# Performance work log

Measured on AMD Instinct MI355X. Metric: run time of the kernel, lower is better.

Reference implementation:

```python
import jax, jax.numpy as jnp
import numpy as np

LEAK = 0.01   # nn.LeakyReLU default negative_slope
EPS = 1e-5    # BatchNorm eps

D, H, W = 32, 480, 480
N = 200000
CIN, COUT = 64, 128


def _neighbor_table(z, y, x, order, sorted_flat, offsets):
    # For each kernel offset, index of the active voxel at (z+dz, y+dy, x+dx), or -1.
    n = z.shape[0]
    tabs = []
    for dz, dy, dx in offsets:
        nz, ny, nx = z + dz, y + dy, x + dx
        valid = (nz >= 0) & (nz < D) & (ny >= 0) & (ny < H) & (nx >= 0) & (nx < W)
        nflat = (nz * H + ny) * W + nx
        pos = np.searchsorted(sorted_flat, nflat).clip(0, n - 1)
        found = valid & (sorted_flat[pos] == nflat)
        tabs.append(np.where(found, order[pos], -1).astype(np.int32))
    return np.stack(tabs)  # [9, N]


def setup_inputs() -> dict:
    rng = np.random.default_rng(0)
    flat = rng.choice(D * H * W, N, replace=False).astype(np.int64)
    z = flat // (H * W)
    y = (flat // W) % H
    x = flat % W
    order = np.argsort(flat)
    sorted_flat = flat[order]
    off133 = [(0, dy, dx) for dy in (-1, 0, 1) for dx in (-1, 0, 1)]  # kernel (1,3,3)
    off313 = [(dz, 0, dx) for dz in (-1, 0, 1) for dx in (-1, 0, 1)]  # kernel (3,1,3)
    nbr133 = jnp.asarray(_neighbor_table(z, y, x, order, sorted_flat, off133))
    nbr313 = jnp.asarray(_neighbor_table(z, y, x, order, sorted_flat, off313))

    key = jax.random.key(0)
    ks = jax.random.split(key, 14)
    feats = jax.random.normal(ks[0], (N, CIN), jnp.float32)
    # SubMConv3d weights, flattened kernel volume first: [9, Cin, Cout]
    W00 = jax.random.normal(ks[1], (9, CIN, COUT), jnp.float32) * 0.05   # conv0_0 (1,3,3)
    W01 = jax.random.normal(ks[2], (9, COUT, COUT), jnp.float32) * 0.05  # conv0_1 (3,1,3)
    W10 = jax.random.normal(ks[3], (9, CIN, COUT), jnp.float32) * 0.05   # conv1_0 (3,1,3)
    W11 = jax.random.normal(ks[4], (9, COUT, COUT), jnp.float32) * 0.05  # conv1_1 (1,3,3)

    def bn_params(k):
        k1, k2, k3, k4 = jax.random.split(k, 4)
        gamma = 1.0 + 0.1 * jax.random.normal(k1, (COUT,), jnp.float32)
        beta = 0.1 * jax.random.normal(k2, (COUT,), jnp.float32)
        mean = 0.1 * jax.random.normal(k3, (COUT,), jnp.float32)
        var = jax.random.uniform(k4, (COUT,), jnp.float32, 0.5, 1.5)
        return jnp.stack([gamma, beta, mean, var])  # [4, Cout]

    return {
        'feats': feats,
        'W00': W00, 'W01': W01, 'W10': W10, 'W11': W11,
        'bn00': bn_params(ks[5]), 'bn01': bn_params(ks[6]),
        'bn10': bn_params(ks[7]), 'bn11': bn_params(ks[8]),
        'nbr133': nbr133, 'nbr313': nbr313,
    }


def _subm_conv(f, nbr, Wk):
    # Rulebook gather-matmul-accumulate: out[n] = sum_k f[nbr[k, n]] @ Wk[k]
    out = jnp.zeros((f.shape[0], Wk.shape[2]), f.dtype)
    for k in range(Wk.shape[0]):  # 9 fixed kernel offsets
        idx = nbr[k]
        valid = idx >= 0
        g = jnp.where(valid[:, None], f[jnp.where(valid, idx, 0)], 0.0)
        out = out + g @ Wk[k]
    return out


def _act_bn(x, p):
    # LeakyReLU then BatchNorm (eval: running stats), matching forward order
    x = jnp.where(x >= 0, x, LEAK * x)
    scale = p[0] * jax.lax.rsqrt(p[3] + EPS)
    return (x - p[2]) * scale + p[1]


def reference(feats, W00, W01, W10, W11, bn00, bn01, bn10, bn11, nbr133, nbr313):
    shortcut = _act_bn(_subm_conv(feats, nbr133, W00), bn00)
    shortcut = _act_bn(_subm_conv(shortcut, nbr313, W01), bn01)
    res = _act_bn(_subm_conv(feats, nbr313, W10), bn10)
    res = _act_bn(_subm_conv(res, nbr133, W11), bn11)
    return res + shortcut
```

## Files before the change

kernel.cpp:

```cpp
#include <hip/hip_runtime.h>
#include <hip/hip_bf16.h>

#define LEAK 0.01f
#define BN_EPS 1e-5f
#define CAP_P 8192

using frag_b16 = __attribute__((ext_vector_type(8))) short;
using f32x4    = __attribute__((ext_vector_type(4))) float;

union U4F { uint4 u; frag_b16 f; };

__device__ __forceinline__ float bf2f(unsigned short u) {
    union { unsigned int i; float f; } v;
    v.i = ((unsigned int)u) << 16;
    return v.f;
}

__device__ __forceinline__ unsigned short f2bf(float f) {
    union { float f; unsigned int i; } v;
    v.f = f;
    unsigned int u = v.i;
    return (unsigned short)((u + 0x7fffu + ((u >> 16) & 1u)) >> 16);
}

__device__ __forceinline__ unsigned int pk_bf16(float lo, float hi) {
    __hip_bfloat162 h = __float22bfloat162_rn(make_float2(lo, hi));
    union { __hip_bfloat162 h; unsigned int u; } c;
    c.h = h;
    return c.u;
}

__global__ __launch_bounds__(256) void transpose_all(
    const float* __restrict__ w0, const float* __restrict__ w1,
    const float* __restrict__ w2, const float* __restrict__ w3,
    const float* __restrict__ b0, const float* __restrict__ b1,
    const float* __restrict__ b2, const float* __restrict__ b3,
    unsigned short* __restrict__ o0, unsigned short* __restrict__ o1,
    unsigned short* __restrict__ o2, unsigned short* __restrict__ o3,
    float* __restrict__ scsh) {
    const int t64 = 9 * 64 * 128, t128 = 9 * 128 * 128;
    int i = blockIdx.x * 256 + threadIdx.x;
    const float* w; unsigned short* o; int cin;
    if (i < t64)                        { w = w0; o = o0; cin = 64; }
    else if ((i -= t64) < t128)         { w = w1; o = o1; cin = 128; }
    else if ((i -= t128) < t64)         { w = w2; o = o2; cin = 64; }
    else if ((i -= t64) < t128)         { w = w3; o = o3; cin = 128; }
    else if ((i -= t128) < 512) {
        int conv = i >> 7, c = i & 127;
        const float* bn = (conv == 0) ? b0 : (conv == 1) ? b1 : (conv == 2) ? b2 : b3;
        float s = bn[c] * rsqrtf(bn[384 + c] + BN_EPS);
        scsh[conv * 256 + c] = s;
        scsh[conv * 256 + 128 + c] = bn[128 + c] - bn[256 + c] * s;
        return;
    }
    else return;
    int co = i & 127;
    int rest = i >> 7;
    int ci = rest % cin;
    int k = rest / cin;
    o[((size_t)k * 128 + co) * cin + ci] = f2bf(w[i]);
}

__global__ __launch_bounds__(256) void rules_count(
    const int* __restrict__ nbrA, const int* __restrict__ nbrB,
    int N, int NB, int* __restrict__ blockCnt) {
    __shared__ int cnts[16][4];
    const int tid = threadIdx.x, lane = tid & 63, wave = tid >> 6;
    const int n = blockIdx.x * 256 + tid;
    #pragma unroll
    for (int c = 0; c < 16; ++c) {
        const int* nb = (c < 8) ? nbrA : nbrB;
        int j = c & 7;
        int k = j + (j >= 4);
        int v = (n < N) ? nb[(size_t)k * N + n] : -1;
        unsigned long long m = __ballot(v >= 0);
        if (lane == 0) cnts[c][wave] = __popcll(m);
    }
    __syncthreads();
    if (tid < 16)
        blockCnt[tid * NB + blockIdx.x] =
            cnts[tid][0] + cnts[tid][1] + cnts[tid][2] + cnts[tid][3];
}

__global__ __launch_bounds__(1024) void rules_scan(
    const int* __restrict__ blockCnt, int NB,
    int* __restrict__ blockBase, int* __restrict__ meta) {
    const int lane = threadIdx.x & 63, w = threadIdx.x >> 6;
    int running = 0;
    for (int base = 0; base < NB; base += 64) {
        int i = base + lane;
        int v = (i < NB) ? blockCnt[w * NB + i] : 0;
        int s = v;
        #pragma unroll
        for (int d = 1; d < 64; d <<= 1) {
            int t = __shfl_up(s, d);
            if (lane >= d) s += t;
        }
        if (i < NB) blockBase[w * NB + i] = running + s - v;
        running += __shfl(s, 63);
    }
    if (lane == 0) meta[w] = running;
}

__global__ __launch_bounds__(256) void rules_fill(
    const int* __restrict__ nbrA, const int* __restrict__ nbrB,
    int N, int NB, const int* __restrict__ blockBase,
    int* __restrict__ pairsAll, int* __restrict__ ptabA, int* __restrict__ ptabB) {
    __shared__ int wcnt[16][4];
    __shared__ int wpre[16][4];
    const int tid = threadIdx.x, lane = tid & 63, wave = tid >> 6;
    const int n = blockIdx.x * 256 + tid;
    int vv[16], rk[16];
    #pragma unroll
    for (int c = 0; c < 16; ++c) {
        const int* nb = (c < 8) ? nbrA : nbrB;
        int j = c & 7;
        int k = j + (j >= 4);
        int v = (n < N) ? nb[(size_t)k * N + n] : -1;
        vv[c] = v;
        unsigned long long m = __ballot(v >= 0);
        rk[c] = (int)__popcll(m & ((1ull << lane) - 1ull));
        if (lane == 0) wcnt[c][wave] = (int)__popcll(m);
    }
    __syncthreads();
    if (tid < 16) {
        int s = 0;
        #pragma unroll
        for (int w = 0; w < 4; ++w) { wpre[tid][w] = s; s += wcnt[tid][w]; }
    }
    __syncthreads();
    if (n < N) {
        #pragma unroll
        for (int c = 0; c < 16; ++c) {
            int j = c & 7;
            int* ptab = (c < 8) ? ptabA : ptabB;
            int idx = -1;
            if (vv[c] >= 0) {
                idx = blockBase[c * NB + blockIdx.x] + wpre[c][wave] + rk[c];
                if (idx < CAP_P) pairsAll[c * CAP_P + idx] = vv[c];
                else idx = -1;
            }
            ptab[(size_t)n * 8 + j] = idx;
        }
    }
}


template <int CIN, bool IN_F32>
__global__ __launch_bounds__(256) void pairs_fused(
    const void* __restrict__ finA, const void* __restrict__ finB,
    const int*  __restrict__ pairsAll,
    const int*  __restrict__ meta,
    const unsigned short* __restrict__ wtA,
    const unsigned short* __restrict__ wtB,
    unsigned short* __restrict__ contribLo,
    unsigned short* __restrict__ contribHi,
    int pairXor) {
    const int job = blockIdx.y;
    const int j = job & 7, k = j + (j >= 4);
    const bool second = job >= 8;
    const void* fin = second ? finB : finA;
    const unsigned short* wk = (second ? wtB : wtA) + (size_t)k * 128 * CIN;
    unsigned short* ctb = (second ? contribHi : contribLo) + (size_t)j * CAP_P * 128;
    const int pidx = job ^ pairXor;
    const int* pairs = pairsAll + (size_t)pidx * CAP_P;
    const int cnt = min(meta[pidx], CAP_P);
    const int wave = threadIdx.x >> 6, lane = threadIdx.x & 63;
    const int l16 = lane & 15, quad = lane >> 4;
    const int pbase = (blockIdx.x * 4 + wave) * 16;
    if (pbase >= cnt) return;
    const int p = pbase + l16;
    const int inrow = (p < cnt) ? pairs[p] : -1;

    f32x4 acc[8] = {};
    #pragma unroll
    for (int c = 0; c < CIN / 32; ++c) {
        U4F u;
        u.u = make_uint4(0u, 0u, 0u, 0u);
        if (inrow >= 0) {
            if (IN_F32) {
                const float* fp = (const float*)fin;
                const float4* p4 = (const float4*)(fp + (size_t)inrow * CIN + c * 32 + quad * 8);
                float4 a = p4[0], b = p4[1];
                u.u.x = pk_bf16(a.x, a.y); u.u.y = pk_bf16(a.z, a.w);
                u.u.z = pk_bf16(b.x, b.y); u.u.w = pk_bf16(b.z, b.w);
            } else {
                u.u = *(const uint4*)((const unsigned short*)fin + (size_t)inrow * CIN + c * 32 + quad * 8);
            }
        }
        frag_b16 bfr = u.f;
        #pragma unroll
        for (int ni = 0; ni < 8; ++ni) {
            frag_b16 afr = *(const frag_b16*)(wk + (size_t)(ni * 16 + l16) * CIN + c * 32 + quad * 8);
            acc[ni] = __builtin_amdgcn_mfma_f32_16x16x32_bf16(afr, bfr, acc[ni], 0, 0, 0);
        }
    }
    if (p < cnt) {
        unsigned short* cr = ctb + (size_t)p * 128 + quad * 4;
        #pragma unroll
        for (int ni = 0; ni < 8; ++ni) {
            uint2 o;
            o.x = pk_bf16(acc[ni][0], acc[ni][1]);
            o.y = pk_bf16(acc[ni][2], acc[ni][3]);
            *(uint2*)(cr + ni * 16) = o;
        }
    }
}

__global__ __launch_bounds__(256, 3) void convK1(
    const float* __restrict__ feats,
    const unsigned short* __restrict__ wt00,
    const unsigned short* __restrict__ wt10,
    const int* __restrict__ ptab133,
    const int* __restrict__ ptab313,
    const unsigned short* __restrict__ contribLo,
    const unsigned short* __restrict__ contribHi,
    const float* __restrict__ scsh,
    unsigned short* __restrict__ s1,
    unsigned short* __restrict__ r1,
    int N) {
    const int tid = threadIdx.x, lane = tid & 63, wave = tid >> 6;
    const int waveM = wave >> 1, waveN = wave & 1;
    const int l16 = lane & 15, quad = lane >> 4;
    const int n0 = blockIdx.x * 64;
    const unsigned short* wS = wt00 + (size_t)4 * 128 * 64;
    const unsigned short* wR = wt10 + (size_t)4 * 128 * 64;

    f32x4 accS[2][4] = {}, accR[2][4] = {};
    #pragma unroll
    for (int c = 0; c < 2; ++c) {
        frag_b16 bF[2];
        #pragma unroll
        for (int mi = 0; mi < 2; ++mi) {
            int n = n0 + waveM * 32 + mi * 16 + l16;
            U4F u;
            u.u = make_uint4(0u, 0u, 0u, 0u);
            if (n < N) {
                const float4* p4 = (const float4*)(feats + (size_t)n * 64 + c * 32 + quad * 8);
                float4 a = p4[0], b = p4[1];
                u.u.x = pk_bf16(a.x, a.y); u.u.y = pk_bf16(a.z, a.w);
                u.u.z = pk_bf16(b.x, b.y); u.u.w = pk_bf16(b.z, b.w);
            }
            bF[mi] = u.f;
        }
        #pragma unroll
        for (int ni = 0; ni < 4; ++ni) {
            frag_b16 aS = *(const frag_b16*)(wS + (size_t)(waveN * 64 + ni * 16 + l16) * 64 + c * 32 + quad * 8);
            frag_b16 aR = *(const frag_b16*)(wR + (size_t)(waveN * 64 + ni * 16 + l16) * 64 + c * 32 + quad * 8);
            #pragma unroll
            for (int mi = 0; mi < 2; ++mi) {
                accS[mi][ni] = __builtin_amdgcn_mfma_f32_16x16x32_bf16(aS, bF[mi], accS[mi][ni], 0, 0, 0);
                accR[mi][ni] = __builtin_amdgcn_mfma_f32_16x16x32_bf16(aR, bF[mi], accR[mi][ni], 0, 0, 0);
            }
        }
    }

    const int cOff = waveN * 64 + quad * 4;
    #pragma unroll
    for (int mi = 0; mi < 2; ++mi) {
        int n = n0 + waveM * 32 + mi * 16 + l16;
        if (n >= N) continue;
        f32x4 mS[4] = {}, mR[4] = {};
        const int4* ptS4 = (const int4*)(ptab133 + (size_t)n * 8);
        const int4* ptR4 = (const int4*)(ptab313 + (size_t)n * 8);
        int4 sa = ptS4[0], sb = ptS4[1];
        int4 ra = ptR4[0], rb = ptR4[1];
        int pjS[8] = {sa.x, sa.y, sa.z, sa.w, sb.x, sb.y, sb.z, sb.w};
        int pjR[8] = {ra.x, ra.y, ra.z, ra.w, rb.x, rb.y, rb.z, rb.w};
        #pragma unroll
        for (int j = 0; j < 8; ++j) {
            if (pjS[j] >= 0) {
                const unsigned short* cr = contribLo + ((size_t)j * CAP_P + pjS[j]) * 128 + cOff;
                #pragma unroll
                for (int ni = 0; ni < 4; ++ni) {
                    uint2 v = *(const uint2*)(cr + ni * 16);
                    mS[ni][0] += bf2f((unsigned short)(v.x & 0xffffu));
                    mS[ni][1] += bf2f((unsigned short)(v.x >> 16));
                    mS[ni][2] += bf2f((unsigned short)(v.y & 0xffffu));
                    mS[ni][3] += bf2f((unsigned short)(v.y >> 16));
                }
            }
            if (pjR[j] >= 0) {
                const unsigned short* cr = contribHi + ((size_t)j * CAP_P + pjR[j]) * 128 + cOff;
                #pragma unroll
                for (int ni = 0; ni < 4; ++ni) {
                    uint2 v = *(const uint2*)(cr + ni * 16);
                    mR[ni][0] += bf2f((unsigned short)(v.x & 0xffffu));
                    mR[ni][1] += bf2f((unsigned short)(v.x >> 16));
                    mR[ni][2] += bf2f((unsigned short)(v.y & 0xffffu));
                    mR[ni][3] += bf2f((unsigned short)(v.y >> 16));
                }
            }
        }
        #pragma unroll
        for (int ni = 0; ni < 4; ++ni) {
            int c = cOff + ni * 16;
            f32x4 scS = *(const f32x4*)(scsh + c);
            f32x4 shS = *(const f32x4*)(scsh + 128 + c);
            f32x4 scR = *(const f32x4*)(scsh + 512 + c);
            f32x4 shR = *(const f32x4*)(scsh + 512 + 128 + c);
            float vs[4], vr[4];
            #pragma unroll
            for (int r = 0; r < 4; ++r) {
                float xs = accS[mi][ni][r] + mS[ni][r];
                xs = (xs >= 0.0f) ? xs : LEAK * xs;
                vs[r] = xs * scS[r] + shS[r];
                float xr = accR[mi][ni][r] + mR[ni][r];
                xr = (xr >= 0.0f) ? xr : LEAK * xr;
                vr[r] = xr * scR[r] + shR[r];
            }
            uint2 oS, oR;
            oS.x = pk_bf16(vs[0], vs[1]); oS.y = pk_bf16(vs[2], vs[3]);
            oR.x = pk_bf16(vr[0], vr[1]); oR.y = pk_bf16(vr[2], vr[3]);
            *(uint2*)(s1 + (size_t)n * 128 + c) = oS;
            *(uint2*)(r1 + (size_t)n * 128 + c) = oR;
        }
    }
}

__global__ __launch_bounds__(256, 3) void convK2(
    const unsigned short* __restrict__ s1,
    const unsigned short* __restrict__ r1,
    const unsigned short* __restrict__ wt01,
    const unsigned short* __restrict__ wt11,
    const int* __restrict__ ptab313,
    const int* __restrict__ ptab133,
    const unsigned short* __restrict__ contribLo,
    const unsigned short* __restrict__ contribHi,
    const float* __restrict__ scsh,
    float* __restrict__ out, int N) {
    const int tid = threadIdx.x, lane = tid & 63, wave = tid >> 6;
    const int waveM = wave >> 1, waveN = wave & 1;
    const int l16 = lane & 15, quad = lane >> 4;
    const int n0 = blockIdx.x * 64;
    const unsigned short* wS = wt01 + (size_t)4 * 128 * 128;
    const unsigned short* wR = wt11 + (size_t)4 * 128 * 128;

    f32x4 accS[2][4] = {}, accR[2][4] = {};
    #pragma unroll
    for (int c = 0; c < 4; ++c) {
        frag_b16 bS[2], bR[2];
        #pragma unroll
        for (int mi = 0; mi < 2; ++mi) {
            int n = n0 + waveM * 32 + mi * 16 + l16;
            U4F us, ur;
            us.u = make_uint4(0u, 0u, 0u, 0u);
            ur.u = us.u;
            if (n < N) {
                us.u = *(const uint4*)(s1 + (size_t)n * 128 + c * 32 + quad * 8);
                ur.u = *(const uint4*)(r1 + (size_t)n * 128 + c * 32 + quad * 8);
            }
            bS[mi] = us.f;
            bR[mi] = ur.f;
        }
        #pragma unroll
        for (int ni = 0; ni < 4; ++ni) {
            frag_b16 aS = *(const frag_b16*)(wS + (size_t)(waveN * 64 + ni * 16 + l16) * 128 + c * 32 + quad * 8);
            frag_b16 aR = *(const frag_b16*)(wR + (size_t)(waveN * 64 + ni * 16 + l16) * 128 + c * 32 + quad * 8);
            #pragma unroll
            for (int mi = 0; mi < 2; ++mi) {
                accS[mi][ni] = __builtin_amdgcn_mfma_f32_16x16x32_bf16(aS, bS[mi], accS[mi][ni], 0, 0, 0);
                accR[mi][ni] = __builtin_amdgcn_mfma_f32_16x16x32_bf16(aR, bR[mi], accR[mi][ni], 0, 0, 0);
            }
        }
    }

    const int cOff = waveN * 64 + quad * 4;
    #pragma unroll
    for (int mi = 0; mi < 2; ++mi) {
        int n = n0 + waveM * 32 + mi * 16 + l16;
        if (n >= N) continue;
        f32x4 mS[4] = {}, mR[4] = {};
        const int4* ptS4 = (const int4*)(ptab313 + (size_t)n * 8);
        const int4* ptR4 = (const int4*)(ptab133 + (size_t)n * 8);
        int4 sa = ptS4[0], sb = ptS4[1];
        int4 ra = ptR4[0], rb = ptR4[1];
        int pjS[8] = {sa.x, sa.y, sa.z, sa.w, sb.x, sb.y, sb.z, sb.w};
        int pjR[8] = {ra.x, ra.y, ra.z, ra.w, rb.x, rb.y, rb.z, rb.w};
        #pragma unroll
        for (int j = 0; j < 8; ++j) {
            if (pjS[j] >= 0) {
                const unsigned short* cr = contribLo + ((size_t)j * CAP_P + pjS[j]) * 128 + cOff;
                #pragma unroll
                for (int ni = 0; ni < 4; ++ni) {
                    uint2 v = *(const uint2*)(cr + ni * 16);
                    mS[ni][0] += bf2f((unsigned short)(v.x & 0xffffu));
                    mS[ni][1] += bf2f((unsigned short)(v.x >> 16));
                    mS[ni][2] += bf2f((unsigned short)(v.y & 0xffffu));
                    mS[ni][3] += bf2f((unsigned short)(v.y >> 16));
                }
            }
            if (pjR[j] >= 0) {
                const unsigned short* cr = contribHi + ((size_t)j * CAP_P + pjR[j]) * 128 + cOff;
                #pragma unroll
                for (int ni = 0; ni < 4; ++ni) {
                    uint2 v = *(const uint2*)(cr + ni * 16);
                    mR[ni][0] += bf2f((unsigned short)(v.x & 0xffffu));
                    mR[ni][1] += bf2f((unsigned short)(v.x >> 16));
                    mR[ni][2] += bf2f((unsigned short)(v.y & 0xffffu));
                    mR[ni][3] += bf2f((unsigned short)(v.y >> 16));
                }
            }
        }
        #pragma unroll
        for (int ni = 0; ni < 4; ++ni) {
            int c = cOff + ni * 16;
            f32x4 sc1 = *(const f32x4*)(scsh + 256 + c);
            f32x4 sh1 = *(const f32x4*)(scsh + 256 + 128 + c);
            f32x4 sc3 = *(const f32x4*)(scsh + 768 + c);
            f32x4 sh3 = *(const f32x4*)(scsh + 768 + 128 + c);
            f32x4 o;
            #pragma unroll
            for (int r = 0; r < 4; ++r) {
                float xs = accS[mi][ni][r] + mS[ni][r];
                xs = (xs >= 0.0f) ? xs : LEAK * xs;
                xs = xs * sc1[r] + sh1[r];
                float xr = accR[mi][ni][r] + mR[ni][r];
                xr = (xr >= 0.0f) ? xr : LEAK * xr;
                xr = xr * sc3[r] + sh3[r];
                o[r] = xr + xs;
            }
            *(f32x4*)(out + (size_t)n * 128 + c) = o;
        }
    }
}


template <int CIN, bool IN_F32>
__global__ __launch_bounds__(256) void pairs_gemm2(
    const void* __restrict__ fin_,
    const int*  __restrict__ pairsT,
    const int*  __restrict__ metaT,
    const unsigned short* __restrict__ wt,
    unsigned short* __restrict__ contrib) {
    const int j = blockIdx.y;
    const int k = j + (j >= 4);
    const int cnt = min(metaT[j], CAP_P);
    const int wave = threadIdx.x >> 6, lane = threadIdx.x & 63;
    const int base = (blockIdx.x * 4 + wave) * 16;
    if (base >= cnt) return;
    const int l16 = lane & 15, quad = lane >> 4;
    const int p = base + l16;
    const int inrow = (p < cnt) ? pairsT[j * CAP_P + p] : -1;
    const unsigned short* wk = wt + (size_t)k * 128 * CIN;

    f32x4 acc[8] = {};
    #pragma unroll
    for (int c = 0; c < CIN / 32; ++c) {
        U4F u;
        u.u = make_uint4(0u, 0u, 0u, 0u);
        if (inrow >= 0) {
            if (IN_F32) {
                const float* fin = (const float*)fin_;
                const float4* p4 = (const float4*)(fin + (size_t)inrow * CIN + c * 32 + quad * 8);
                float4 a = p4[0], b = p4[1];
                u.u.x = pk_bf16(a.x, a.y); u.u.y = pk_bf16(a.z, a.w);
                u.u.z = pk_bf16(b.x, b.y); u.u.w = pk_bf16(b.z, b.w);
            } else {
                u.u = *(const uint4*)((const unsigned short*)fin_ + (size_t)inrow * CIN + c * 32 + quad * 8);
            }
        }
        frag_b16 af = u.f;
        #pragma unroll
        for (int ni = 0; ni < 8; ++ni) {
            frag_b16 bf = *(const frag_b16*)(wk + (ni * 16 + l16) * CIN + c * 32 + quad * 8);
            acc[ni] = __builtin_amdgcn_mfma_f32_16x16x32_bf16(af, bf, acc[ni], 0, 0, 0);
        }
    }
    unsigned short* cj = contrib + ((size_t)j * CAP_P + base) * 128;
    #pragma unroll
    for (int r = 0; r < 4; ++r) {
        int row = quad * 4 + r;
        #pragma unroll
        for (int ni = 0; ni < 8; ++ni)
            cj[(size_t)row * 128 + ni * 16 + l16] = f2bf(acc[ni][r]);
    }
}

template <int CIN, bool IN_F32, bool OUT_BF16, int ADDMODE>
__global__ __launch_bounds__(256, 4) void conv_center3(
    const void* __restrict__ fin_,
    const unsigned short* __restrict__ wt,
    const int*  __restrict__ ptabT,
    const unsigned short* __restrict__ contrib,
    const float* __restrict__ bn,
    const unsigned short* __restrict__ addbf,
    void* __restrict__ out_,
    int N) {
    const int tid = threadIdx.x;
    const int lane = tid & 63;
    const int wave = tid >> 6;
    const int waveM = wave >> 1, waveN = wave & 1;
    const int l16 = lane & 15, quad = lane >> 4;
    const int n0 = blockIdx.x * 64;
    const unsigned short* wc = wt + (size_t)4 * 128 * CIN;

    f32x4 acc[2][4] = {};
    #pragma unroll
    for (int c = 0; c < CIN / 32; ++c) {
        frag_b16 bf[4], af[2];
        #pragma unroll
        for (int ni = 0; ni < 4; ++ni)
            bf[ni] = *(const frag_b16*)(wc + (waveN * 64 + ni * 16 + l16) * CIN + c * 32 + quad * 8);
        #pragma unroll
        for (int mi = 0; mi < 2; ++mi) {
            int n = n0 + waveM * 32 + mi * 16 + l16;
            U4F u;
            u.u = make_uint4(0u, 0u, 0u, 0u);
            if (n < N) {
                if (IN_F32) {
                    const float* fin = (const float*)fin_;
                    const float4* p4 = (const float4*)(fin + (size_t)n * CIN + c * 32 + quad * 8);
                    float4 a = p4[0], b = p4[1];
                    u.u.x = pk_bf16(a.x, a.y); u.u.y = pk_bf16(a.z, a.w);
                    u.u.z = pk_bf16(b.x, b.y); u.u.w = pk_bf16(b.z, b.w);
                } else {
                    u.u = *(const uint4*)((const unsigned short*)fin_ + (size_t)n * CIN + c * 32 + quad * 8);
                }
            }
            af[mi] = u.f;
        }
        #pragma unroll
        for (int mi = 0; mi < 2; ++mi)
            #pragma unroll
            for (int ni = 0; ni < 4; ++ni)
                acc[mi][ni] = __builtin_amdgcn_mfma_f32_16x16x32_bf16(af[mi], bf[ni], acc[mi][ni], 0, 0, 0);
    }

    float sc[4], sh[4];
    int col[4];
    #pragma unroll
    for (int ni = 0; ni < 4; ++ni) {
        int c = waveN * 64 + ni * 16 + l16;
        col[ni] = c;
        float s = bn[c] * rsqrtf(bn[384 + c] + BN_EPS);
        sc[ni] = s;
        sh[ni] = bn[128 + c] - bn[256 + c] * s;
    }
    #pragma unroll
    for (int mi = 0; mi < 2; ++mi) {
        int rbase = n0 + waveM * 32 + mi * 16 + quad * 4;
        #pragma unroll
        for (int r = 0; r < 4; ++r) {
            int n = rbase + r;
            if (n < N) {
                const int4* pt = (const int4*)(ptabT + (size_t)n * 8);
                int4 pa = pt[0], pb = pt[1];
                int pj[8] = {pa.x, pa.y, pa.z, pa.w, pb.x, pb.y, pb.z, pb.w};
                float m[4] = {0.f, 0.f, 0.f, 0.f};
                #pragma unroll
                for (int j = 0; j < 8; ++j) {
                    int pi = pj[j];
                    if (pi >= 0) {
                        const unsigned short* cr = contrib + ((size_t)j * CAP_P + pi) * 128;
                        #pragma unroll
                        for (int ni = 0; ni < 4; ++ni) m[ni] += bf2f(cr[col[ni]]);
                    }
                }
                float addv[4] = {0.f, 0.f, 0.f, 0.f};
                if (ADDMODE == 1) {
                    #pragma unroll
                    for (int ni = 0; ni < 4; ++ni)
                        addv[ni] = bf2f(addbf[(size_t)n * 128 + col[ni]]);
                } else if (ADDMODE == 2) {
                    #pragma unroll
                    for (int ni = 0; ni < 4; ++ni)
                        addv[ni] = ((const float*)out_)[(size_t)n * 128 + col[ni]];
                }
                #pragma unroll
                for (int ni = 0; ni < 4; ++ni) {
                    float x = acc[mi][ni][r] + m[ni];
                    x = (x >= 0.0f) ? x : LEAK * x;
                    x = x * sc[ni] + sh[ni];
                    x += addv[ni];
                    if (OUT_BF16)
                        ((unsigned short*)out_)[(size_t)n * 128 + col[ni]] = f2bf(x);
                    else
                        ((float*)out_)[(size_t)n * 128 + col[ni]] = x;
                }
            }
        }
    }
}

template <int CIN, bool IN_F32, bool OUT_F32, bool ADD>
__global__ __launch_bounds__(256) void conv_mfma(
    const void*  __restrict__ fin_,
    const int*   __restrict__ nbr,
    const unsigned short* __restrict__ wt,
    const float* __restrict__ bn,
    const float* __restrict__ addsrc,
    void*        __restrict__ out_,
    int N) {
    constexpr int SEGS = CIN / 8;
    constexpr int RPP = 256 / SEGS;
    constexpr int PASSES = 128 / RPP;
    __shared__ unsigned short ldsA[128 * CIN];
    __shared__ unsigned short ldsW[128 * CIN];
    const int tid = threadIdx.x;
    const int lane = tid & 63;
    const int wave = tid >> 6;
    const int waveM = wave >> 1, waveN = wave & 1;
    const int l16 = lane & 15, quad = lane >> 4;
    const int n0 = blockIdx.x * 128;
    const int srow = tid / SEGS, sseg = tid % SEGS;
    f32x4 acc[4][4] = {};
    for (int k = 0; k < 9; ++k) {
        if (k) __syncthreads();
        #pragma unroll
        for (int p = 0; p < PASSES; ++p) {
            int r = p * RPP + srow;
            int n = n0 + r;
            int idx = (n < N) ? nbr[(size_t)k * N + n] : -1;
            uint4 v = make_uint4(0u, 0u, 0u, 0u);
            if (IN_F32) {
                const float* fin = (const float*)fin_;
                float4 a = make_float4(0.f, 0.f, 0.f, 0.f);
                float4 b = make_float4(0.f, 0.f, 0.f, 0.f);
                if (idx >= 0) {
                    const float4* p4 = (const float4*)(fin + (size_t)idx * CIN) + sseg * 2;
                    a = p4[0]; b = p4[1];
                }
                v.x = pk_bf16(a.x, a.y); v.y = pk_bf16(a.z, a.w);
                v.z = pk_bf16(b.x, b.y); v.w = pk_bf16(b.z, b.w);
            } else {
                const unsigned short* fin = (const unsigned short*)fin_;
                if (idx >= 0) v = *((const uint4*)(fin + (size_t)idx * CIN) + sseg);
            }
            *(uint4*)(ldsA + r * CIN + ((sseg ^ (r & 7)) << 3)) = v;
        }
        const unsigned short* wk = wt + (size_t)k * 128 * CIN;
        #pragma unroll
        for (int p = 0; p < PASSES; ++p) {
            int r = p * RPP + srow;
            *(uint4*)(ldsW + r * CIN + ((sseg ^ (r & 7)) << 3)) =
                *((const uint4*)(wk + r * CIN) + sseg);
        }
        __syncthreads();
        #pragma unroll
        for (int c = 0; c < CIN / 32; ++c) {
            frag_b16 af[4], bf[4];
            #pragma unroll
            for (int i = 0; i < 4; ++i) {
                int seg = (c * 4 + quad) ^ (l16 & 7);
                af[i] = *(const frag_b16*)(ldsA + (waveM * 64 + i * 16 + l16) * CIN + (seg << 3));
                bf[i] = *(const frag_b16*)(ldsW + (waveN * 64 + i * 16 + l16) * CIN + (seg << 3));
            }
            #pragma unroll
            for (int mi = 0; mi < 4; ++mi)
                #pragma unroll
                for (int ni = 0; ni < 4; ++ni)
                    acc[mi][ni] = __builtin_amdgcn_mfma_f32_16x16x32_bf16(af[mi], bf[ni], acc[mi][ni], 0, 0, 0);
        }
    }
    float sc[4], sh[4];
    int col[4];
    #pragma unroll
    for (int ni = 0; ni < 4; ++ni) {
        int c = waveN * 64 + ni * 16 + l16;
        col[ni] = c;
        float s = bn[c] * rsqrtf(bn[384 + c] + BN_EPS);
        sc[ni] = s;
        sh[ni] = bn[128 + c] - bn[256 + c] * s;
    }
    #pragma unroll
    for (int mi = 0; mi < 4; ++mi) {
        int rbase = n0 + waveM * 64 + mi * 16 + quad * 4;
        #pragma unroll
        for (int r = 0; r < 4; ++r) {
            int n = rbase + r;
            if (n < N) {
                #pragma unroll
                for (int ni = 0; ni < 4; ++ni) {
                    float x = acc[mi][ni][r];
                    x = (x >= 0.0f) ? x : LEAK * x;
                    x = x * sc[ni] + sh[ni];
                    if (ADD) x += addsrc[(size_t)n * 128 + col[ni]];
                    if (OUT_F32) ((float*)out_)[(size_t)n * 128 + col[ni]] = x;
                    else ((unsigned short*)out_)[(size_t)n * 128 + col[ni]] = f2bf(x);
                }
            }
        }
    }
}

extern "C" void kernel_launch(void* const* d_in, const int* in_sizes, int n_in,
                              void* d_out, int out_size, void* d_ws, size_t ws_size,
                              hipStream_t stream) {
    const float* feats = (const float*)d_in[0];
    const float* W00 = (const float*)d_in[1];
    const float* W01 = (const float*)d_in[2];
    const float* W10 = (const float*)d_in[3];
    const float* W11 = (const float*)d_in[4];
    const float* bn00 = (const float*)d_in[5];
    const float* bn01 = (const float*)d_in[6];
    const float* bn10 = (const float*)d_in[7];
    const float* bn11 = (const float*)d_in[8];
    const int* nbr133 = (const int*)d_in[9];
    const int* nbr313 = (const int*)d_in[10];
    const int N = in_sizes[0] / 64;
    const int NB = (N + 255) / 256;

    char* ws = (char*)d_ws;
    size_t off = 0;
    auto alloc = [&](size_t bytes) -> char* {
        char* p = ws + off;
        off = (off + bytes + 255) & ~(size_t)255;
        return p;
    };
    unsigned short* bufA = (unsigned short*)alloc((size_t)N * 128 * 2);
    unsigned short* wt00 = (unsigned short*)alloc(9 * 128 * 64 * 2);
    unsigned short* wt01 = (unsigned short*)alloc(9 * 128 * 128 * 2);
    unsigned short* wt10 = (unsigned short*)alloc(9 * 128 * 64 * 2);
    unsigned short* wt11 = (unsigned short*)alloc(9 * 128 * 128 * 2);
    float* scsh = (float*)alloc(4 * 2 * 128 * 4);
    int* ptab133 = (int*)alloc((size_t)N * 8 * 4);
    int* ptab313 = (int*)alloc((size_t)N * 8 * 4);
    int* pairsAll = (int*)alloc((size_t)16 * CAP_P * 4);
    int* blockCnt = (int*)alloc((size_t)16 * NB * 4);
    int* blockBase = (int*)alloc((size_t)16 * NB * 4);
    int* meta = (int*)alloc(16 * 4);
    unsigned short* contribLo = (unsigned short*)alloc((size_t)8 * CAP_P * 128 * 2);
    const size_t offTierB = off;
    unsigned short* bufB = (unsigned short*)alloc((size_t)N * 128 * 2);
    const size_t offTierA = off;
    unsigned short* contribHi = (unsigned short*)alloc((size_t)8 * CAP_P * 128 * 2);
    const size_t offFused = off;

    const bool fusedOk = (ws_size >= offFused);
    const bool tierA = (ws_size >= offTierA);
    const bool tierB = (ws_size >= offTierB);

    const int totalW = 2 * (9 * 64 * 128) + 2 * (9 * 128 * 128);
    hipLaunchKernelGGL(transpose_all, dim3((totalW + 512 + 255) / 256), dim3(256), 0, stream,
                       W00, W01, W10, W11, bn00, bn01, bn10, bn11,
                       wt00, wt01, wt10, wt11, scsh);

    float* outF = (float*)d_out;
    const int cblocks = (N + 63) / 64;

    if (fusedOk) {
        hipLaunchKernelGGL(rules_count, dim3(NB), dim3(256), 0, stream,
                           nbr133, nbr313, N, NB, blockCnt);
        hipLaunchKernelGGL(rules_scan, dim3(1), dim3(1024), 0, stream,
                           blockCnt, NB, blockBase, meta);
        hipLaunchKernelGGL(rules_fill, dim3(NB), dim3(256), 0, stream,
                           nbr133, nbr313, N, NB, blockBase, pairsAll, ptab133, ptab313);

        const dim3 pg(CAP_P / 64, 16);
        hipLaunchKernelGGL((pairs_fused<64, true>), pg, dim3(256), 0, stream,
                           (const void*)feats, (const void*)feats, pairsAll, meta,
                           wt00, wt10, contribLo, contribHi, 0);
        hipLaunchKernelGGL(convK1, dim3(cblocks), dim3(256), 0, stream,
                           feats, wt00, wt10, ptab133, ptab313,
                           contribLo, contribHi, scsh, bufA, bufB, N);
        hipLaunchKernelGGL((pairs_fused<128, false>), pg, dim3(256), 0, stream,
                           (const void*)bufA, (const void*)bufB, pairsAll, meta,
                           wt01, wt11, contribLo, contribHi, 8);
        hipLaunchKernelGGL(convK2, dim3(cblocks), dim3(256), 0, stream,
                           bufA, bufB, wt01, wt11, ptab313, ptab133,
                           contribLo, contribHi, scsh, outF, N);
    } else if (tierA || tierB) {
        hipLaunchKernelGGL(rules_count, dim3(NB), dim3(256), 0, stream,
                           nbr133, nbr313, N, NB, blockCnt);
        hipLaunchKernelGGL(rules_scan, dim3(1), dim3(1024), 0, stream,
                           blockCnt, NB, blockBase, meta);
        hipLaunchKernelGGL(rules_fill, dim3(NB), dim3(256), 0, stream,
                           nbr133, nbr313, N, NB, blockBase, pairsAll, ptab133, ptab313);

        const dim3 pg(CAP_P / 64, 8);
        const int* pairs133 = pairsAll;
        const int* pairs313 = pairsAll + 8 * CAP_P;
        const int* meta133 = meta;
        const int* meta313 = meta + 8;
        const unsigned short* nullbf = nullptr;

        hipLaunchKernelGGL((pairs_gemm2<64, true>), pg, dim3(256), 0, stream,
                           (const void*)feats, pairs133, meta133, wt00, contribLo);
        hipLaunchKernelGGL((conv_center3<64, true, true, 0>), dim3(cblocks), dim3(256), 0, stream,
                           (const void*)feats, wt00, ptab133, contribLo, bn00, nullbf, (void*)bufA, N);
        hipLaunchKernelGGL((pairs_gemm2<128, false>), pg, dim3(256), 0, stream,
                           (const void*)bufA, pairs313, meta313, wt01, contribLo);
        if (tierA)
            hipLaunchKernelGGL((conv_center3<128, false, true, 0>), dim3(cblocks), dim3(256), 0, stream,
                               (const void*)bufA, wt01, ptab313, contribLo, bn01, nullbf, (void*)bufB, N);
        else
            hipLaunchKernelGGL((conv_center3<128, false, false, 0>), dim3(cblocks), dim3(256), 0, stream,
                               (const void*)bufA, wt01, ptab313, contribLo, bn01, nullbf, (void*)outF, N);
        hipLaunchKernelGGL((pairs_gemm2<64, true>), pg, dim3(256), 0, stream,
                           (const void*)feats, pairs313, meta313, wt10, contribLo);
        hipLaunchKernelGGL((conv_center3<64, true, true, 0>), dim3(cblocks), dim3(256), 0, stream,
                           (const void*)feats, wt10, ptab313, contribLo, bn10, nullbf, (void*)bufA, N);
        hipLaunchKernelGGL((pairs_gemm2<128, false>), pg, dim3(256), 0, stream,
                           (const void*)bufA, pairs133, meta133, wt11, contribLo);
        if (tierA)
            hipLaunchKernelGGL((conv_center3<128, false, false, 1>), dim3(cblocks), dim3(256), 0, stream,
                               (const void*)bufA, wt11, ptab133, contribLo, bn11, bufB, (void*)outF, N);
        else
            hipLaunchKernelGGL((conv_center3<128, false, false, 2>), dim3(cblocks), dim3(256), 0, stream,
                               (const void*)bufA, wt11, ptab133, contribLo, bn11, nullbf, (void*)outF, N);
    } else {
        const int blocks = (N + 127) / 128;
        hipLaunchKernelGGL((conv_mfma<64, true, false, false>), dim3(blocks), dim3(256), 0, stream,
                           (const void*)feats, nbr133, wt00, bn00, (const float*)nullptr, (void*)bufA, N);
        hipLaunchKernelGGL((conv_mfma<128, false, true, false>), dim3(blocks), dim3(256), 0, stream,
                           (const void*)bufA, nbr313, wt01, bn01, (const float*)nullptr, (void*)outF, N);
        hipLaunchKernelGGL((conv_mfma<64, true, false, false>), dim3(blocks), dim3(256), 0, stream,
                           (const void*)feats, nbr313, wt10, bn10, (const float*)nullptr, (void*)bufA, N);
        hipLaunchKernelGGL((conv_mfma<128, false, true, true>), dim3(blocks), dim3(256), 0, stream,
                           (const void*)bufA, nbr133, wt11, bn11, outF, (void*)outF, N);
    }
}
```

Measured before the change: 460.3 us.

## Pack neighbor pair lists compactly, shrink conv tiles, pre-convert feats to bf16

Replaces the per-voxel 8-int pair tables with a packed 16-byte list of valid (offset, pair index) entries, so the center conv kernels read one uint4 and loop only over present neighbors instead of checking eight entries. The fused conv kernels now process 32 voxels per block with higher occupancy (launch bounds 4) and do the neighbor merge before the MFMA loop. When workspace allows, feats are converted once to bf16 so the pair GEMM and first center conv read half the bytes. This costs an extra conversion kernel and restructured workspace allocation, and halves per-block weight reuse.

```diff
diff --git a/kernel.cpp b/kernel.cpp
--- a/kernel.cpp
+++ b/kernel.cpp
@@ -61,6 +61,18 @@
     o[((size_t)k * 128 + co) * cin + ci] = f2bf(w[i]);
 }
 
+__global__ __launch_bounds__(256) void feats_to_bf16(
+    const float* __restrict__ f, unsigned short* __restrict__ o, int total8) {
+    int i = blockIdx.x * 256 + threadIdx.x;
+    if (i >= total8) return;
+    const float4* p4 = (const float4*)(f + (size_t)i * 8);
+    float4 a = p4[0], b = p4[1];
+    uint4 u;
+    u.x = pk_bf16(a.x, a.y); u.y = pk_bf16(a.z, a.w);
+    u.z = pk_bf16(b.x, b.y); u.w = pk_bf16(b.z, b.w);
+    ((uint4*)o)[i] = u;
+}
+
 __global__ __launch_bounds__(256) void rules_count(
     const int* __restrict__ nbrA, const int* __restrict__ nbrB,
     int N, int NB, int* __restrict__ blockCnt) {
@@ -105,7 +117,9 @@
 __global__ __launch_bounds__(256) void rules_fill(
     const int* __restrict__ nbrA, const int* __restrict__ nbrB,
     int N, int NB, const int* __restrict__ blockBase,
-    int* __restrict__ pairsAll, int* __restrict__ ptabA, int* __restrict__ ptabB) {
+    int* __restrict__ pairsAll,
+    int* __restrict__ ptabA, int* __restrict__ ptabB,
+    uint4* __restrict__ pakA, uint4* __restrict__ pakB) {
     __shared__ int wcnt[16][4];
     __shared__ int wpre[16][4];
     const int tid = threadIdx.x, lane = tid & 63, wave = tid >> 6;
@@ -130,18 +144,42 @@
     }
     __syncthreads();
     if (n < N) {
+        unsigned long long la0 = ~0ull, la1 = ~0ull, lb0 = ~0ull, lb1 = ~0ull;
+        int na = 0, nbp = 0;
         #pragma unroll
         for (int c = 0; c < 16; ++c) {
             int j = c & 7;
-            int* ptab = (c < 8) ? ptabA : ptabB;
             int idx = -1;
             if (vv[c] >= 0) {
                 idx = blockBase[c * NB + blockIdx.x] + wpre[c][wave] + rk[c];
                 if (idx < CAP_P) pairsAll[c * CAP_P + idx] = vv[c];
                 else idx = -1;
             }
-            ptab[(size_t)n * 8 + j] = idx;
-        }
+            if (c < 8) { if (ptabA) ptabA[(size_t)n * 8 + j] = idx; }
+            else       { if (ptabB) ptabB[(size_t)n * 8 + j] = idx; }
+            if (idx >= 0) {
+                unsigned e = ((unsigned)j << 13) | (unsigned)idx;
+                if (e != 0xFFFFu) {
+                    if (c < 8) {
+                        int s = (na & 3) * 16;
+                        unsigned long long m = 0xFFFFull << s;
+                        unsigned long long ev = (unsigned long long)e << s;
+                        if (na < 4) la0 = (la0 & ~m) | ev; else la1 = (la1 & ~m) | ev;
+                        ++na;
+                    } else {
+                        int s = (nbp & 3) * 16;
+                        unsigned long long m = 0xFFFFull << s;
+                        unsigned long long ev = (unsigned long long)e << s;
+                        if (nbp < 4) lb0 = (lb0 & ~m) | ev; else lb1 = (lb1 & ~m) | ev;
+                        ++nbp;
+                    }
+                }
+            }
+        }
+        if (pakA) pakA[n] = make_uint4((unsigned)la0, (unsigned)(la0 >> 32),
+                                       (unsigned)la1, (unsigned)(la1 >> 32));
+        if (pakB) pakB[n] = make_uint4((unsigned)lb0, (unsigned)(lb0 >> 32),
+                                       (unsigned)lb1, (unsigned)(lb1 >> 32));
     }
 }
 
@@ -207,12 +245,35 @@
     }
 }
 
-__global__ __launch_bounds__(256, 3) void convK1(
-    const float* __restrict__ feats,
+__device__ __forceinline__ void merge_gather(
+    uint4 pk, const unsigned short* __restrict__ contrib, int cOff, f32x4 (&acc)[4]) {
+    if (pk.x == 0xFFFFFFFFu) return;
+    unsigned long long lo = ((unsigned long long)pk.y << 32) | pk.x;
+    unsigned long long hi = ((unsigned long long)pk.w << 32) | pk.z;
+    #pragma unroll 1
+    for (int t = 0; t < 8; ++t) {
+        unsigned v = (unsigned)(((t < 4) ? lo : hi) >> ((t & 3) << 4)) & 0xFFFFu;
+        if (v == 0xFFFFu) break;
+        const unsigned short* cr =
+            contrib + ((size_t)(v >> 13) * CAP_P + (v & 0x1FFFu)) * 128 + cOff;
+        #pragma unroll
+        for (int ni = 0; ni < 4; ++ni) {
+            uint2 g = *(const uint2*)(cr + ni * 16);
+            acc[ni][0] += bf2f((unsigned short)(g.x & 0xffffu));
+            acc[ni][1] += bf2f((unsigned short)(g.x >> 16));
+            acc[ni][2] += bf2f((unsigned short)(g.y & 0xffffu));
+            acc[ni][3] += bf2f((unsigned short)(g.y >> 16));
+        }
+    }
+}
+
+template <bool IN_F32>
+__global__ __launch_bounds__(256, 4) void convK1(
+    const void* __restrict__ feats_,
     const unsigned short* __restrict__ wt00,
     const unsigned short* __restrict__ wt10,
-    const int* __restrict__ ptab133,
-    const int* __restrict__ ptab313,
+    const uint4* __restrict__ pakA,
+    const uint4* __restrict__ pakB,
     const unsigned short* __restrict__ contribLo,
     const unsigned short* __restrict__ contribHi,
     const float* __restrict__ scsh,
@@ -222,90 +283,56 @@
     const int tid = threadIdx.x, lane = tid & 63, wave = tid >> 6;
     const int waveM = wave >> 1, waveN = wave & 1;
     const int l16 = lane & 15, quad = lane >> 4;
-    const int n0 = blockIdx.x * 64;
+    const int n = blockIdx.x * 32 + waveM * 16 + l16;
+    const bool live = (n < N);
     const unsigned short* wS = wt00 + (size_t)4 * 128 * 64;
     const unsigned short* wR = wt10 + (size_t)4 * 128 * 64;
-
-    f32x4 accS[2][4] = {}, accR[2][4] = {};
+    const int cOff = waveN * 64 + quad * 4;
+
+    f32x4 accS[4] = {}, accR[4] = {};
+    if (live) {
+        merge_gather(pakA[n], contribLo, cOff, accS);
+        merge_gather(pakB[n], contribHi, cOff, accR);
+    }
     #pragma unroll
     for (int c = 0; c < 2; ++c) {
-        frag_b16 bF[2];
-        #pragma unroll
-        for (int mi = 0; mi < 2; ++mi) {
-            int n = n0 + waveM * 32 + mi * 16 + l16;
-            U4F u;
-            u.u = make_uint4(0u, 0u, 0u, 0u);
-            if (n < N) {
-                const float4* p4 = (const float4*)(feats + (size_t)n * 64 + c * 32 + quad * 8);
+        U4F u;
+        u.u = make_uint4(0u, 0u, 0u, 0u);
+        if (live) {
+            if (IN_F32) {
+                const float* fp = (const float*)feats_;
+                const float4* p4 = (const float4*)(fp + (size_t)n * 64 + c * 32 + quad * 8);
                 float4 a = p4[0], b = p4[1];
                 u.u.x = pk_bf16(a.x, a.y); u.u.y = pk_bf16(a.z, a.w);
                 u.u.z = pk_bf16(b.x, b.y); u.u.w = pk_bf16(b.z, b.w);
-            }
-            bF[mi] = u.f;
-        }
+            } else {
+                u.u = *(const uint4*)((const unsigned short*)feats_ + (size_t)n * 64 + c * 32 + quad * 8);
+            }
+        }
+        frag_b16 bIn = u.f;
         #pragma unroll
         for (int ni = 0; ni < 4; ++ni) {
             frag_b16 aS = *(const frag_b16*)(wS + (size_t)(waveN * 64 + ni * 16 + l16) * 64 + c * 32 + quad * 8);
             frag_b16 aR = *(const frag_b16*)(wR + (size_t)(waveN * 64 + ni * 16 + l16) * 64 + c * 32 + quad * 8);
-            #pragma unroll
-            for (int mi = 0; mi < 2; ++mi) {
-                accS[mi][ni] = __builtin_amdgcn_mfma_f32_16x16x32_bf16(aS, bF[mi], accS[mi][ni], 0, 0, 0);
-                accR[mi][ni] = __builtin_amdgcn_mfma_f32_16x16x32_bf16(aR, bF[mi], accR[mi][ni], 0, 0, 0);
-            }
-        }
-    }
-
-    const int cOff = waveN * 64 + quad * 4;
-    #pragma unroll
-    for (int mi = 0; mi < 2; ++mi) {
-        int n = n0 + waveM * 32 + mi * 16 + l16;
-        if (n >= N) continue;
-        f32x4 mS[4] = {}, mR[4] = {};
-        const int4* ptS4 = (const int4*)(ptab133 + (size_t)n * 8);
-        const int4* ptR4 = (const int4*)(ptab313 + (size_t)n * 8);
-        int4 sa = ptS4[0], sb = ptS4[1];
-        int4 ra = ptR4[0], rb = ptR4[1];
-        int pjS[8] = {sa.x, sa.y, sa.z, sa.w, sb.x, sb.y, sb.z, sb.w};
-        int pjR[8] = {ra.x, ra.y, ra.z, ra.w, rb.x, rb.y, rb.z, rb.w};
-        #pragma unroll
-        for (int j = 0; j < 8; ++j) {
-            if (pjS[j] >= 0) {
-                const unsigned short* cr = contribLo + ((size_t)j * CAP_P + pjS[j]) * 128 + cOff;
-                #pragma unroll
-                for (int ni = 0; ni < 4; ++ni) {
-                    uint2 v = *(const uint2*)(cr + ni * 16);
-                    mS[ni][0] += bf2f((unsigned short)(v.x & 0xffffu));
-                    mS[ni][1] += bf2f((unsigned short)(v.x >> 16));
-                    mS[ni][2] += bf2f((unsigned short)(v.y & 0xffffu));
-                    mS[ni][3] += bf2f((unsigned short)(v.y >> 16));
-                }
-            }
-            if (pjR[j] >= 0) {
-                const unsigned short* cr = contribHi + ((size_t)j * CAP_P + pjR[j]) * 128 + cOff;
-                #pragma unroll
-                for (int ni = 0; ni < 4; ++ni) {
-                    uint2 v = *(const uint2*)(cr + ni * 16);
-                    mR[ni][0] += bf2f((unsigned short)(v.x & 0xffffu));
-                    mR[ni][1] += bf2f((unsigned short)(v.x >> 16));
-                    mR[ni][2] += bf2f((unsigned short)(v.y & 0xffffu));
-                    mR[ni][3] += bf2f((unsigned short)(v.y >> 16));
-                }
-            }
-        }
+            accS[ni] = __builtin_amdgcn_mfma_f32_16x16x32_bf16(aS, bIn, accS[ni], 0, 0, 0);
+            accR[ni] = __builtin_amdgcn_mfma_f32_16x16x32_bf16(aR, bIn, accR[ni], 0, 0, 0);
+        }
+    }
+    if (live) {
         #pragma unroll
         for (int ni = 0; ni < 4; ++ni) {
             int c = cOff + ni * 16;
             f32x4 scS = *(const f32x4*)(scsh + c);
             f32x4 shS = *(const f32x4*)(scsh + 128 + c);
             f32x4 scR = *(const f32x4*)(scsh + 512 + c);
-            f32x4 shR = *(const f32x4*)(scsh + 512 + 128 + c);
+            f32x4 shR = *(const f32x4*)(scsh + 640 + c);
             float vs[4], vr[4];
             #pragma unroll
             for (int r = 0; r < 4; ++r) {
-                float xs = accS[mi][ni][r] + mS[ni][r];
+                float xs = accS[ni][r];
                 xs = (xs >= 0.0f) ? xs : LEAK * xs;
                 vs[r] = xs * scS[r] + shS[r];
-                float xr = accR[mi][ni][r] + mR[ni][r];
+                float xr = accR[ni][r];
                 xr = (xr >= 0.0f) ? xr : LEAK * xr;
                 vr[r] = xr * scR[r] + shR[r];
             }
@@ -318,13 +345,13 @@
     }
 }
 
-__global__ __launch_bounds__(256, 3) void convK2(
+__global__ __launch_bounds__(256, 4) void convK2(
     const unsigned short* __restrict__ s1,
     const unsigned short* __restrict__ r1,
     const unsigned short* __restrict__ wt01,
     const unsigned short* __restrict__ wt11,
-    const int* __restrict__ ptab313,
-    const int* __restrict__ ptab133,
+    const uint4* __restrict__ pakB,
+    const uint4* __restrict__ pakA,
     const unsigned short* __restrict__ contribLo,
     const unsigned short* __restrict__ contribHi,
     const float* __restrict__ scsh,
@@ -332,90 +359,50 @@
     const int tid = threadIdx.x, lane = tid & 63, wave = tid >> 6;
     const int waveM = wave >> 1, waveN = wave & 1;
     const int l16 = lane & 15, quad = lane >> 4;
-    const int n0 = blockIdx.x * 64;
+    const int n = blockIdx.x * 32 + waveM * 16 + l16;
+    const bool live = (n < N);
     const unsigned short* wS = wt01 + (size_t)4 * 128 * 128;
     const unsigned short* wR = wt11 + (size_t)4 * 128 * 128;
-
-    f32x4 accS[2][4] = {}, accR[2][4] = {};
+    const int cOff = waveN * 64 + quad * 4;
+
+    f32x4 accS[4] = {}, accR[4] = {};
+    if (live) {
+        merge_gather(pakB[n], contribLo, cOff, accS);
+        merge_gather(pakA[n], contribHi, cOff, accR);
+    }
     #pragma unroll
     for (int c = 0; c < 4; ++c) {
-        frag_b16 bS[2], bR[2];
-        #pragma unroll
-        for (int mi = 0; mi < 2; ++mi) {
-            int n = n0 + waveM * 32 + mi * 16 + l16;
-            U4F us, ur;
-            us.u = make_uint4(0u, 0u, 0u, 0u);
-            ur.u = us.u;
-            if (n < N) {
-                us.u = *(const uint4*)(s1 + (size_t)n * 128 + c * 32 + quad * 8);
-                ur.u = *(const uint4*)(r1 + (size_t)n * 128 + c * 32 + quad * 8);
-            }
-            bS[mi] = us.f;
-            bR[mi] = ur.f;
-        }
+        U4F us, ur;
+        us.u = make_uint4(0u, 0u, 0u, 0u);
+        ur.u = us.u;
+        if (live) {
+            us.u = *(const uint4*)(s1 + (size_t)n * 128 + c * 32 + quad * 8);
+            ur.u = *(const uint4*)(r1 + (size_t)n * 128 + c * 32 + quad * 8);
+        }
+        frag_b16 bS = us.f, bR = ur.f;
         #pragma unroll
         for (int ni = 0; ni < 4; ++ni) {
             frag_b16 aS = *(const frag_b16*)(wS + (size_t)(waveN * 64 + ni * 16 + l16) * 128 + c * 32 + quad * 8);
             frag_b16 aR = *(const frag_b16*)(wR + (size_t)(waveN * 64 + ni * 16 + l16) * 128 + c * 32 + quad * 8);
-            #pragma unroll
-            for (int mi = 0; mi < 2; ++mi) {
-                accS[mi][ni] = __builtin_amdgcn_mfma_f32_16x16x32_bf16(aS, bS[mi], accS[mi][ni], 0, 0, 0);
-                accR[mi][ni] = __builtin_amdgcn_mfma_f32_16x16x32_bf16(aR, bR[mi], accR[mi][ni], 0, 0, 0);
-            }
-        }
-    }
-
-    const int cOff = waveN * 64 + quad * 4;
-    #pragma unroll
-    for (int mi = 0; mi < 2; ++mi) {
-        int n = n0 + waveM * 32 + mi * 16 + l16;
-        if (n >= N) continue;
-        f32x4 mS[4] = {}, mR[4] = {};
-        const int4* ptS4 = (const int4*)(ptab313 + (size_t)n * 8);
-        const int4* ptR4 = (const int4*)(ptab133 + (size_t)n * 8);
-        int4 sa = ptS4[0], sb = ptS4[1];
-        int4 ra = ptR4[0], rb = ptR4[1];
-        int pjS[8] = {sa.x, sa.y, sa.z, sa.w, sb.x, sb.y, sb.z, sb.w};
-        int pjR[8] = {ra.x, ra.y, ra.z, ra.w, rb.x, rb.y, rb.z, rb.w};
-        #pragma unroll
-        for (int j = 0; j < 8; ++j) {
-            if (pjS[j] >= 0) {
-                const unsigned short* cr = contribLo + ((size_t)j * CAP_P + pjS[j]) * 128 + cOff;
-                #pragma unroll
-                for (int ni = 0; ni < 4; ++ni) {
-                    uint2 v = *(const uint2*)(cr + ni * 16);
-                    mS[ni][0] += bf2f((unsigned short)(v.x & 0xffffu));
-                    mS[ni][1] += bf2f((unsigned short)(v.x >> 16));
-                    mS[ni][2] += bf2f((unsigned short)(v.y & 0xffffu));
-                    mS[ni][3] += bf2f((unsigned short)(v.y >> 16));
-                }
-            }
-            if (pjR[j] >= 0) {
-                const unsigned short* cr = contribHi + ((size_t)j * CAP_P + pjR[j]) * 128 + cOff;
-                #pragma unroll
-                for (int ni = 0; ni < 4; ++ni) {
-                    uint2 v = *(const uint2*)(cr + ni * 16);
-                    mR[ni][0] += bf2f((unsigned short)(v.x & 0xffffu));
-                    mR[ni][1] += bf2f((unsigned short)(v.x >> 16));
-                    mR[ni][2] += bf2f((unsigned short)(v.y & 0xffffu));
-                    mR[ni][3] += bf2f((unsigned short)(v.y >> 16));
-                }
-            }
-        }
+            accS[ni] = __builtin_amdgcn_mfma_f32_16x16x32_bf16(aS, bS, accS[ni], 0, 0, 0);
+            accR[ni] = __builtin_amdgcn_mfma_f32_16x16x32_bf16(aR, bR, accR[ni], 0, 0, 0);
+        }
+    }
+    if (live) {
         #pragma unroll
         for (int ni = 0; ni < 4; ++ni) {
             int c = cOff + ni * 16;
             f32x4 sc1 = *(const f32x4*)(scsh + 256 + c);
-            f32x4 sh1 = *(const f32x4*)(scsh + 256 + 128 + c);
+            f32x4 sh1 = *(const f32x4*)(scsh + 384 + c);
             f32x4 sc3 = *(const f32x4*)(scsh + 768 + c);
-            f32x4 sh3 = *(const f32x4*)(scsh + 768 + 128 + c);
+            f32x4 sh3 = *(const f32x4*)(scsh + 896 + c);
             f32x4 o;
             #pragma unroll
             for (int r = 0; r < 4; ++r) {
-                float xs = accS[mi][ni][r] + mS[ni][r];
+                float xs = accS[ni][r];
                 xs = (xs >= 0.0f) ? xs : LEAK * xs;
                 xs = xs * sc1[r] + sh1[r];
-                float xr = accR[mi][ni][r] + mR[ni][r];
+                float xr = accR[ni][r];
                 xr = (xr >= 0.0f) ? xr : LEAK * xr;
                 xr = xr * sc3[r] + sh3[r];
                 o[r] = xr + xs;
@@ -714,20 +701,30 @@
     unsigned short* wt10 = (unsigned short*)alloc(9 * 128 * 64 * 2);
     unsigned short* wt11 = (unsigned short*)alloc(9 * 128 * 128 * 2);
     float* scsh = (float*)alloc(4 * 2 * 128 * 4);
-    int* ptab133 = (int*)alloc((size_t)N * 8 * 4);
-    int* ptab313 = (int*)alloc((size_t)N * 8 * 4);
     int* pairsAll = (int*)alloc((size_t)16 * CAP_P * 4);
     int* blockCnt = (int*)alloc((size_t)16 * NB * 4);
     int* blockBase = (int*)alloc((size_t)16 * NB * 4);
     int* meta = (int*)alloc(16 * 4);
     unsigned short* contribLo = (unsigned short*)alloc((size_t)8 * CAP_P * 128 * 2);
-    const size_t offTierB = off;
+    const size_t offX = off;
+
+    uint4* pakA = (uint4*)alloc((size_t)N * 16);
+    uint4* pakB = (uint4*)alloc((size_t)N * 16);
     unsigned short* bufB = (unsigned short*)alloc((size_t)N * 128 * 2);
-    const size_t offTierA = off;
     unsigned short* contribHi = (unsigned short*)alloc((size_t)8 * CAP_P * 128 * 2);
     const size_t offFused = off;
+    unsigned short* feats16 = (unsigned short*)alloc((size_t)N * 64 * 2);
+    const size_t offFusedF16 = off;
+
+    off = offX;
+    int* ptab133 = (int*)alloc((size_t)N * 8 * 4);
+    int* ptab313 = (int*)alloc((size_t)N * 8 * 4);
+    const size_t offTierB = off;
+    unsigned short* bufB_t = (unsigned short*)alloc((size_t)N * 128 * 2);
+    const size_t offTierA = off;
 
     const bool fusedOk = (ws_size >= offFused);
+    const bool useF16 = (ws_size >= offFusedF16);
     const bool tierA = (ws_size >= offTierA);
     const bool tierB = (ws_size >= offTierB);
 
@@ -737,28 +734,43 @@
                        wt00, wt01, wt10, wt11, scsh);
 
     float* outF = (float*)d_out;
-    const int cblocks = (N + 63) / 64;
 
     if (fusedOk) {
+        if (useF16) {
+            const int total8 = N * 8;
+            hipLaunchKernelGGL(feats_to_bf16, dim3((total8 + 255) / 256), dim3(256), 0, stream,
+                               feats, feats16, total8);
+        }
         hipLaunchKernelGGL(rules_count, dim3(NB), dim3(256), 0, stream,
                            nbr133, nbr313, N, NB, blockCnt);
         hipLaunchKernelGGL(rules_scan, dim3(1), dim3(1024), 0, stream,
                            blockCnt, NB, blockBase, meta);
         hipLaunchKernelGGL(rules_fill, dim3(NB), dim3(256), 0, stream,
-                           nbr133, nbr313, N, NB, blockBase, pairsAll, ptab133, ptab313);
+                           nbr133, nbr313, N, NB, blockBase, pairsAll,
+                           (int*)nullptr, (int*)nullptr, pakA, pakB);
 
         const dim3 pg(CAP_P / 64, 16);
-        hipLaunchKernelGGL((pairs_fused<64, true>), pg, dim3(256), 0, stream,
-                           (const void*)feats, (const void*)feats, pairsAll, meta,
-                           wt00, wt10, contribLo, contribHi, 0);
-        hipLaunchKernelGGL(convK1, dim3(cblocks), dim3(256), 0, stream,
-                           feats, wt00, wt10, ptab133, ptab313,
-                           contribLo, contribHi, scsh, bufA, bufB, N);
+        const int kblocks = (N + 31) / 32;
+        if (useF16) {
+            hipLaunchKernelGGL((pairs_fused<64, false>), pg, dim3(256), 0, stream,
+                               (const void*)feats16, (const void*)feats16, pairsAll, meta,
+                               wt00, wt10, contribLo, contribHi, 0);
+            hipLaunchKernelGGL((convK1<false>), dim3(kblocks), dim3(256), 0, stream,
+                               (const void*)feats16, wt00, wt10, pakA, pakB,
+                               contribLo, contribHi, scsh, bufA, bufB, N);
+        } else {
+            hipLaunchKernelGGL((pairs_fused<64, true>), pg, dim3(256), 0, stream,
+                               (const void*)feats, (const void*)feats, pairsAll, meta,
+                               wt00, wt10, contribLo, contribHi, 0);
+            hipLaunchKernelGGL((convK1<true>), dim3(kblocks), dim3(256), 0, stream,
+                               (const void*)feats, wt00, wt10, pakA, pakB,
+                               contribLo, contribHi, scsh, bufA, bufB, N);
+        }
         hipLaunchKernelGGL((pairs_fused<128, false>), pg, dim3(256), 0, stream,
                            (const void*)bufA, (const void*)bufB, pairsAll, meta,
                            wt01, wt11, contribLo, contribHi, 8);
-        hipLaunchKernelGGL(convK2, dim3(cblocks), dim3(256), 0, stream,
-                           bufA, bufB, wt01, wt11, ptab313, ptab133,
+        hipLaunchKernelGGL(convK2, dim3(kblocks), dim3(256), 0, stream,
+                           bufA, bufB, wt01, wt11, pakB, pakA,
                            contribLo, contribHi, scsh, outF, N);
     } else if (tierA || tierB) {
         hipLaunchKernelGGL(rules_count, dim3(NB), dim3(256), 0, stream,
@@ -766,7 +778,8 @@
         hipLaunchKernelGGL(rules_scan, dim3(1), dim3(1024), 0, stream,
                            blockCnt, NB, blockBase, meta);
         hipLaunchKernelGGL(rules_fill, dim3(NB), dim3(256), 0, stream,
-                           nbr133, nbr313, N, NB, blockBase, pairsAll, ptab133, ptab313);
+                           nbr133, nbr313, N, NB, blockBase, pairsAll,
+                           ptab133, ptab313, (uint4*)nullptr, (uint4*)nullptr);
 
         const dim3 pg(CAP_P / 64, 8);
         const int* pairs133 = pairsAll;
@@ -774,6 +787,7 @@
         const int* meta133 = meta;
         const int* meta313 = meta + 8;
         const unsigned short* nullbf = nullptr;
+        const int cblocks = (N + 63) / 64;
 
         hipLaunchKernelGGL((pairs_gemm2<64, true>), pg, dim3(256), 0, stream,
                            (const void*)feats, pairs133, meta133, wt00, contribLo);
@@ -783,7 +797,7 @@
                            (const void*)bufA, pairs313, meta313, wt01, contribLo);
         if (tierA)
             hipLaunchKernelGGL((conv_center3<128, false, true, 0>), dim3(cblocks), dim3(256), 0, stream,
-                               (const void*)bufA, wt01, ptab313, contribLo, bn01, nullbf, (void*)bufB, N);
+                               (const void*)bufA, wt01, ptab313, contribLo, bn01, nullbf, (void*)bufB_t, N);
         else
             hipLaunchKernelGGL((conv_center3<128, false, false, 0>), dim3(cblocks), dim3(256), 0, stream,
                                (const void*)bufA, wt01, ptab313, contribLo, bn01, nullbf, (void*)outF, N);
@@ -795,7 +809,7 @@
                            (const void*)bufA, pairs133, meta133, wt11, contribLo);
         if (tierA)
             hipLaunchKernelGGL((conv_center3<128, false, false, 1>), dim3(cblocks), dim3(256), 0, stream,
-                               (const void*)bufA, wt11, ptab133, contribLo, bn11, bufB, (void*)outF, N);
+                               (const void*)bufA, wt11, ptab133, contribLo, bn11, bufB_t, (void*)outF, N);
         else
             hipLaunchKernelGGL((conv_center3<128, false, false, 2>), dim3(cblocks), dim3(256), 0, stream,
                                (const void*)bufA, wt11, ptab133, contribLo, bn11, nullbf, (void*)outF, N);
```

New measurement: 482.6 us. 1.05x slower.
